# Kernel optimization log

Hardware: AMD Instinct MI355X
Metric: run time of the kernel (lower is better)

The kernel has to match this reference:

```python
import jax, jax.numpy as jnp
import numpy as np

B, T, C = 4, 2048, 1024
N_HEADS = 16
HEAD_DIM = C // N_HEADS


def setup_inputs() -> dict:
    key = jax.random.key(0)
    k1, k2, k3, k4, k5 = jax.random.split(key, 5)
    x = jax.random.normal(k1, (B, T, C), dtype=jnp.float32)
    # torch Linear: y = x @ W.T + b; store W as [out, in]
    w_qkv = jax.random.normal(k2, (3 * C, C), dtype=jnp.float32) * (1.0 / np.sqrt(C))
    b_qkv = jax.random.normal(k3, (3 * C,), dtype=jnp.float32) * 0.01
    w_proj = jax.random.normal(k4, (C, C), dtype=jnp.float32) * (1.0 / np.sqrt(C))
    b_proj = jax.random.normal(k5, (C,), dtype=jnp.float32) * 0.01
    return {"x": x, "w_qkv": w_qkv, "b_qkv": b_qkv, "w_proj": w_proj, "b_proj": b_proj}


def reference(x, w_qkv, b_qkv, w_proj, b_proj):
    Bx, Tx, Cx = x.shape
    scale = 1.0 / np.sqrt(HEAD_DIM)
    qkv = x @ w_qkv.T + b_qkv                              # [B,T,3C]
    qkv = qkv.reshape(Bx, Tx, 3, N_HEADS, HEAD_DIM)
    qkv = jnp.transpose(qkv, (2, 0, 3, 1, 4))              # [3,B,H,T,D]
    q, k, v = qkv[0], qkv[1], qkv[2]
    att = jnp.einsum('bhqd,bhkd->bhqk', q, k) * scale      # [B,H,T,T]
    causal = jnp.tril(jnp.ones((Tx, Tx), dtype=bool))
    att = jnp.where(causal[None, None, :, :], att, -jnp.inf)
    att = jax.nn.softmax(att, axis=-1)
    # dropout p=0.0 (eval) -> identity
    out = jnp.einsum('bhqk,bhkd->bhqd', att, v)            # [B,H,T,D]
    out = jnp.transpose(out, (0, 2, 1, 3)).reshape(Bx, Tx, Cx)
    return out @ w_proj.T + b_proj
```

## Files before the change

### kernel.cpp

```cpp
#include <hip/hip_runtime.h>
#include <hip/hip_bf16.h>
#include <cstdint>

typedef __attribute__((ext_vector_type(8))) short bf16x8;
typedef __attribute__((ext_vector_type(4))) float f32x4;
typedef __attribute__((ext_vector_type(16))) float f32x16;

#define MFMA16(a, b, c) __builtin_amdgcn_mfma_f32_16x16x32_bf16(a, b, c, 0, 0, 0)
#define MFMA32(a, b, c) __builtin_amdgcn_mfma_f32_32x32x16_bf16(a, b, c, 0, 0, 0)

typedef __attribute__((address_space(1))) uint32_t as1_u32;
typedef __attribute__((address_space(3))) uint32_t as3_u32;
static __device__ __forceinline__ void gload16(const void* g, void* l) {
  __builtin_amdgcn_global_load_lds((as1_u32*)g, (as3_u32*)l, 16, 0, 0);
}

static __device__ __forceinline__ ushort f2b(float f) {
  union { float f; uint32_t u; } v; v.f = f;
  uint32_t u = v.u;
  uint32_t r = (u + 0x7FFFu + ((u >> 16) & 1u)) >> 16;
  return (ushort)r;
}

static __device__ __forceinline__ uint32_t cvtpk(float a, float b) {
  uint32_t r;
  asm("v_cvt_pk_bf16_f32 %0, %1, %2" : "=v"(r) : "v"(a), "v"(b));
  return r;
}
static __device__ __forceinline__ void plswap(uint32_t& a, uint32_t& b) {
  asm volatile("v_permlane32_swap_b32 %0, %1" : "+v"(a), "+v"(b));
}

#define QSCALE 0.1803368782f

#define LOFF(r, kc4) (((r) >> 1) * 64 + ((((((r) & 1) << 2) | (kc4)) ^ (((r) >> 1) & 7)) * 8))

__global__ void cvt_f32_bf16(const float* __restrict__ in, ushort* __restrict__ out, int n4) {
  int i = blockIdx.x * blockDim.x + threadIdx.x;
  if (i >= n4) return;
  const float4 v = ((const float4*)in)[i];
  ushort4 o;
  o.x = f2b(v.x); o.y = f2b(v.y); o.z = f2b(v.z); o.w = f2b(v.w);
  ((ushort4*)out)[i] = o;
}

__global__ __launch_bounds__(512, 2) void gemm_qkv_8ph(
    const ushort* __restrict__ A,
    const ushort* __restrict__ W,
    const float* __restrict__ bias,
    int M, int N, int K,
    ushort* __restrict__ q_ws, ushort* __restrict__ k_ws, ushort* __restrict__ v_ws) {
  __shared__ ushort As[2][2][64 * 64];
  __shared__ ushort Bs[2][2][2][64 * 64];
  const int tid = threadIdx.x;
  const int cpx = gridDim.x >> 3;
  const int wg = (blockIdx.x & 7) * cpx + (blockIdx.x >> 3);
  const int m0 = (wg / 12) * 128, n0 = (wg % 12) * 256;
  const int wid = tid >> 6, lane = tid & 63;
  const int wr = wid >> 2, wc = wid & 3;
  const int lr = lane & 15, lg = lane >> 4;
  const int prow = tid >> 3, pchk = tid & 7;
  const int lchk = pchk ^ (prow & 7);
  const int srow = prow * 2 + (lchk >> 2);
  const int skc = (lchk & 3) * 8;

  f32x4 acc[4][4] = {};
  const int nt = K >> 6;

#define STA(db_, kt_)                                                         \
  { const ushort* src = A + (size_t)(m0 + srow) * K + (kt_)*64 + skc;         \
    gload16(src, &As[db_][0][tid * 8]);                                       \
    gload16(src + 32, &As[db_][1][tid * 8]); }
#define STB(db_, half_, kt_)                                                  \
  { const ushort* src = W + (size_t)(n0 + (half_)*128 + srow) * K + (kt_)*64 + skc; \
    gload16(src, &Bs[db_][half_][0][tid * 8]);                                \
    gload16(src + 32, &Bs[db_][half_][1][tid * 8]); }

  STB(0, 0, 0); STB(0, 1, 0);
  STA(0, 0);
  STB(1, 0, 1); STB(1, 1, 1);
  asm volatile("s_waitcnt vmcnt(4)" ::: "memory");
  __builtin_amdgcn_s_barrier();

  const int bhalf = wc >> 1, brow = (wc & 1) * 64;
  for (int T = 0; T < nt; ++T) {
    const int db = T & 1;
    const ushort* Asub0 = &As[db][0][0];
    const ushort* Asub1 = &As[db][1][0];
    const ushort* Bsub0 = &Bs[db][bhalf][0][0];
    const ushort* Bsub1 = &Bs[db][bhalf][1][0];
    bf16x8 b[4][2];
    {
      bf16x8 a[2][2];
#pragma unroll
      for (int mm = 0; mm < 2; ++mm) {
        const int r = wr * 64 + mm * 16 + lr;
        a[mm][0] = *(const bf16x8*)&Asub0[LOFF(r, lg)];
        a[mm][1] = *(const bf16x8*)&Asub1[LOFF(r, lg)];
      }
#pragma unroll
      for (int nf = 0; nf < 4; ++nf) {
        const int r = brow + nf * 16 + lr;
        b[nf][0] = *(const bf16x8*)&Bsub0[LOFF(r, lg)];
        b[nf][1] = *(const bf16x8*)&Bsub1[LOFF(r, lg)];
      }
      if (T + 1 < nt) STA((T + 1) & 1, T + 1);
      __builtin_amdgcn_sched_barrier(0);
      __builtin_amdgcn_s_barrier();
      asm volatile("s_waitcnt lgkmcnt(0)" ::: "memory");
      __builtin_amdgcn_sched_barrier(0);
      __builtin_amdgcn_s_setprio(1);
#pragma unroll
      for (int kk = 0; kk < 2; ++kk)
#pragma unroll
        for (int mm = 0; mm < 2; ++mm)
#pragma unroll
          for (int nf = 0; nf < 4; ++nf)
            acc[mm][nf] = MFMA16(a[mm][kk], b[nf][kk], acc[mm][nf]);
      __builtin_amdgcn_s_setprio(0);
      __builtin_amdgcn_s_barrier();
    }
    {
      bf16x8 a[2][2];
#pragma unroll
      for (int mm = 0; mm < 2; ++mm) {
        const int r = wr * 64 + (2 + mm) * 16 + lr;
        a[mm][0] = *(const bf16x8*)&Asub0[LOFF(r, lg)];
        a[mm][1] = *(const bf16x8*)&Asub1[LOFF(r, lg)];
      }
      if (T + 2 < nt) { STB(db, 0, T + 2); STB(db, 1, T + 2); }
      __builtin_amdgcn_sched_barrier(0);
      __builtin_amdgcn_s_barrier();
      asm volatile("s_waitcnt lgkmcnt(0)" ::: "memory");
      __builtin_amdgcn_sched_barrier(0);
      __builtin_amdgcn_s_setprio(1);
#pragma unroll
      for (int kk = 0; kk < 2; ++kk)
#pragma unroll
        for (int mm = 0; mm < 2; ++mm)
#pragma unroll
          for (int nf = 0; nf < 4; ++nf)
            acc[2 + mm][nf] = MFMA16(a[mm][kk], b[nf][kk], acc[2 + mm][nf]);
      __builtin_amdgcn_s_setprio(0);
      if (T + 2 < nt)
        asm volatile("s_waitcnt vmcnt(4)" ::: "memory");
      else if (T + 1 < nt)
        asm volatile("s_waitcnt vmcnt(0)" ::: "memory");
      if (T + 1 < nt) __builtin_amdgcn_s_barrier();
    }
  }
#undef STA
#undef STB

#pragma unroll
  for (int mf = 0; mf < 4; ++mf) {
#pragma unroll
    for (int nf = 0; nf < 4; ++nf) {
      const int rowb = m0 + wr * 64 + mf * 16 + lg * 4;
      const int col = n0 + wc * 64 + nf * 16 + lr;
      float v[4];
#pragma unroll
      for (int i = 0; i < 4; ++i) v[i] = acc[mf][nf][i] + bias[col];
      const int sel = col >> 10;
      const int rem = col & 1023;
      const int h = rem >> 6, d = rem & 63;
      const int bb = rowb >> 11, t0 = rowb & 2047;
      if (sel == 2) {
        ushort4 st;
        st.x = f2b(v[0]); st.y = f2b(v[1]); st.z = f2b(v[2]); st.w = f2b(v[3]);
        *(ushort4*)&v_ws[((size_t)(bb * 16 + h) * 64 + d) * 2048 + t0] = st;
      } else if (sel == 0) {
#pragma unroll
        for (int i = 0; i < 4; ++i)
          q_ws[((size_t)(bb * 16 + h) * 2048 + t0 + i) * 64 + d] = f2b(v[i] * QSCALE);
      } else {
#pragma unroll
        for (int i = 0; i < 4; ++i)
          k_ws[((size_t)(bb * 16 + h) * 2048 + t0 + i) * 64 + d] = f2b(v[i]);
      }
    }
  }
}

__global__ __launch_bounds__(256) void gemm_proj(
    const ushort* __restrict__ A,
    const ushort* __restrict__ W,
    const float* __restrict__ bias,
    int M, int N, int K,
    float* __restrict__ out) {
  __shared__ ushort As[3][64 * 64];
  __shared__ ushort Bs[3][64 * 64];
  const int tid = threadIdx.x;
  const int nbx = N >> 7;
  const int cpx = gridDim.x >> 3;
  const int wg = (blockIdx.x & 7) * cpx + (blockIdx.x >> 3);
  const int m0 = (wg / nbx) * 128, n0 = (wg % nbx) * 128;
  const int lane = tid & 63, w = tid >> 6;
  const int lr = lane & 15, lg = lane >> 4;
  const int wm = (w >> 1) * 64, wn = (w & 1) * 64;
  f32x4 acc[4][4] = {};

  const int nt = K >> 5;

#define GSTAGE(buf_, kt_)                                                   \
  do {                                                                      \
    const ushort* Asrc = A + (size_t)m0 * K + (kt_) * 32;                   \
    const ushort* Bsrc = W + (size_t)n0 * K + (kt_) * 32;                   \
    _Pragma("unroll") for (int i_ = 0; i_ < 2; ++i_) {                      \
      const int ch = i_ * 256 + tid;                                        \
      const int prow = ch >> 3, pchk = ch & 7;                              \
      const int lchk = pchk ^ (prow & 7);                                   \
      const int r = prow * 2 + (lchk >> 2), kc = (lchk & 3) * 8;            \
      gload16(&Asrc[(size_t)r * K + kc], &As[buf_][ch * 8]);                \
      gload16(&Bsrc[(size_t)r * K + kc], &Bs[buf_][ch * 8]);                \
    }                                                                       \
  } while (0)

  GSTAGE(0, 0);
  GSTAGE(1, 1);
  asm volatile("s_waitcnt vmcnt(4)" ::: "memory");
  __builtin_amdgcn_s_barrier();
  asm volatile("" ::: "memory");

  int bcur = 0, bnxt = 2;
  for (int t = 0; t < nt; ++t) {
    if (t + 2 < nt) GSTAGE(bnxt, t + 2);
    const ushort* Asc = As[bcur];
    const ushort* Bsc = Bs[bcur];
    bf16x8 a[4], b[4];
#pragma unroll
    for (int mi = 0; mi < 4; ++mi) {
      const int r = wm + mi * 16 + lr;
      a[mi] = *(const bf16x8*)&Asc[LOFF(r, lg)];
    }
#pragma unroll
    for (int ni = 0; ni < 4; ++ni) {
      const int r = wn + ni * 16 + lr;
      b[ni] = *(const bf16x8*)&Bsc[LOFF(r, lg)];
    }
    __builtin_amdgcn_s_setprio(1);
#pragma unroll
    for (int mi = 0; mi < 4; ++mi)
#pragma unroll
      for (int ni = 0; ni < 4; ++ni)
        acc[mi][ni] = MFMA16(a[mi], b[ni], acc[mi][ni]);
    __builtin_amdgcn_s_setprio(0);
    if (t + 2 < nt)
      asm volatile("s_waitcnt vmcnt(4)" ::: "memory");
    else if (t + 1 < nt)
      asm volatile("s_waitcnt vmcnt(0)" ::: "memory");
    if (t + 1 < nt) {
      __builtin_amdgcn_s_barrier();
      asm volatile("" ::: "memory");
    }
    bcur = (bcur == 2) ? 0 : bcur + 1;
    bnxt = (bnxt == 2) ? 0 : bnxt + 1;
  }
#undef GSTAGE

#pragma unroll
  for (int mi = 0; mi < 4; ++mi) {
#pragma unroll
    for (int ni = 0; ni < 4; ++ni) {
      const int rowb = m0 + wm + mi * 16 + lg * 4;
      const int col = n0 + wn + ni * 16 + lr;
#pragma unroll
      for (int i = 0; i < 4; ++i)
        out[(size_t)(rowb + i) * N + col] = acc[mi][ni][i] + bias[col];
    }
  }
}

__global__ __launch_bounds__(256) void attn_v5(
    const ushort* __restrict__ Q, const ushort* __restrict__ K,
    const ushort* __restrict__ VT, ushort* __restrict__ O ) {
  const int blk = blockIdx.x;
  const int bh = blk & 63;
  const int pr = blk >> 6;
  const int tid = threadIdx.x;
  const int w = tid >> 6, lane = tid & 63;
  const int l31 = lane & 31, l5 = lane >> 5;
  const int bb = bh >> 4, h = bh & 15;
  const size_t base = (size_t)bh * 2048 * 64;
  const ushort* Qb = Q + base;
  const ushort* Kb = K + base;
  const ushort* VTb = VT + base;

  __shared__ ushort Ks[2][64 * 64];
  __shared__ ushort Vs[2][64 * 64];
  __shared__ float l_lds[4][32];

#define STAGE(buf, kt_)                                              \
  do {                                                               \
    const ushort* Kt = Kb + (size_t)(kt_) * 64 * 64;                 \
    const ushort* Vt = VTb + (kt_) * 64;                             \
    _Pragma("unroll") for (int i_ = 0; i_ < 2; ++i_) {               \
      const int ch = i_ * 256 + tid;                                 \
      const int r = ch >> 3;                                         \
      const int csw = ((ch & 7) ^ (r & 7)) * 8;                      \
      gload16(&Kt[(size_t)r * 64 + csw], &Ks[buf][ch * 8]);          \
      gload16(&Vt[(size_t)r * 2048 + csw], &Vs[buf][ch * 8]);        \
    }                                                                \
  } while (0)

#pragma unroll 1
  for (int ph = 0; ph < 2; ++ph) {
    const int s = ph ? pr : 15 - pr;
    const int q0w = s * 128 + w * 32;
    const int nt = 2 * s + 2;
    const int qlane = q0w + l31;

    bf16x8 qf[4];
#pragma unroll
    for (int dblk = 0; dblk < 4; ++dblk)
      qf[dblk] = *(const bf16x8*)&Qb[(size_t)qlane * 64 + dblk * 16 + l5 * 8];

    f32x16 o0 = {}, o1 = {};
    float lsum = 0.f;

    STAGE(0, 0);
    __syncthreads();

    for (int kt = 0; kt < nt; ++kt) {
      const int cur = kt & 1;
      if (kt + 1 < nt) STAGE(cur ^ 1, kt + 1);
      const int k0 = kt << 6;
      const ushort* Ksc = Ks[cur];
      const ushort* Vsc = Vs[cur];
#pragma unroll
      for (int kblk = 0; kblk < 2; ++kblk) {
        const int kbase = k0 + kblk * 32;
        if (kbase <= q0w + 31) {
          f32x16 st = {};
          __builtin_amdgcn_s_setprio(1);
#pragma unroll
          for (int dblk = 0; dblk < 4; ++dblk) {
            const int row = kblk * 32 + l31;
            bf16x8 ka = *(const bf16x8*)&Ksc[row * 64 + (((dblk * 2 + l5) ^ (row & 7)) * 8)];
            st = MFMA32(ka, qf[dblk], st);
          }
          __builtin_amdgcn_s_setprio(0);
          if (kbase + 31 > q0w) {
#pragma unroll
            for (int r = 0; r < 16; ++r) {
              const int kk = kbase + (r & 3) + 8 * (r >> 2) + 4 * l5;
              st[r] = (kk <= qlane) ? st[r] : -INFINITY;
            }
          }
          float p[16];
#pragma unroll
          for (int r = 0; r < 16; ++r) {
            p[r] = __builtin_amdgcn_exp2f(st[r]);
            lsum += p[r];
          }
#pragma unroll
          for (int sbl = 0; sbl < 2; ++sbl) {
            uint32_t P0 = cvtpk(p[8 * sbl + 0], p[8 * sbl + 1]);
            uint32_t P1 = cvtpk(p[8 * sbl + 2], p[8 * sbl + 3]);
            uint32_t P2 = cvtpk(p[8 * sbl + 4], p[8 * sbl + 5]);
            uint32_t P3 = cvtpk(p[8 * sbl + 6], p[8 * sbl + 7]);
            plswap(P0, P2);
            plswap(P1, P3);
            union { uint32_t u[4]; bf16x8 v; } pk;
            pk.u[0] = P0; pk.u[1] = P1; pk.u[2] = P2; pk.u[3] = P3;
            const int kchunk = kblk * 4 + sbl * 2 + l5;
            __builtin_amdgcn_s_setprio(1);
#pragma unroll
            for (int db2 = 0; db2 < 2; ++db2) {
              const int vrow = db2 * 32 + l31;
              bf16x8 vb = *(const bf16x8*)&Vsc[vrow * 64 + ((kchunk ^ (vrow & 7)) * 8)];
              if (db2 == 0) o0 = MFMA32(pk.v, vb, o0);
              else          o1 = MFMA32(pk.v, vb, o1);
            }
            __builtin_amdgcn_s_setprio(0);
          }
        }
      }
      __syncthreads();
    }

    const float lfull = lsum + __shfl_xor(lsum, 32);
    if (lane < 32) l_lds[w][lane] = 1.f / lfull;
#pragma unroll
    for (int r = 0; r < 16; ++r) {
      const int qoff = (r & 3) + 8 * (r >> 2) + 4 * l5;
      const float inv = l_lds[w][qoff];
      const int t = q0w + qoff;
      ushort* op = &O[(size_t)(bb * 2048 + t) * 1024 + h * 64 + l31];
      op[0] = f2b(o0[r] * inv);
      op[32] = f2b(o1[r] * inv);
    }
  }
#undef STAGE
}

extern "C" void kernel_launch(void* const* d_in, const int* in_sizes, int n_in,
                              void* d_out, int out_size, void* d_ws, size_t ws_size,
                              hipStream_t stream) {
  const float* x = (const float*)d_in[0];
  const float* w_qkv = (const float*)d_in[1];
  const float* b_qkv = (const float*)d_in[2];
  const float* w_proj = (const float*)d_in[3];
  const float* b_proj = (const float*)d_in[4];
  float* out = (float*)d_out;

  char* ws = (char*)d_ws;
  const size_t SZ_X = (size_t)8192 * 1024 * 2;
  const size_t SZ_WQ = (size_t)3072 * 1024 * 2;
  const size_t SZ_WP = (size_t)1024 * 1024 * 2;
  ushort* xb = (ushort*)(ws);
  ushort* wqb = (ushort*)(ws + SZ_X);
  ushort* wpb = (ushort*)(ws + SZ_X + SZ_WQ);
  ushort* q_ws = (ushort*)(ws + SZ_X + SZ_WQ + SZ_WP);
  ushort* k_ws = q_ws + (size_t)8192 * 1024;
  ushort* v_ws = k_ws + (size_t)8192 * 1024;

  cvt_f32_bf16<<<8388608 / 4 / 256, 256, 0, stream>>>(x, xb, 8388608 / 4);
  cvt_f32_bf16<<<3145728 / 4 / 256, 256, 0, stream>>>(w_qkv, wqb, 3145728 / 4);
  cvt_f32_bf16<<<1048576 / 4 / 256, 256, 0, stream>>>(w_proj, wpb, 1048576 / 4);

  gemm_qkv_8ph<<<768, 512, 0, stream>>>(
      xb, wqb, b_qkv, 8192, 3072, 1024, q_ws, k_ws, v_ws);

  attn_v5<<<512, 256, 0, stream>>>(q_ws, k_ws, v_ws, xb);

  gemm_proj<<<512, 256, 0, stream>>>(
      xb, wpb, b_proj, 8192, 1024, 1024, out);
}
```

Baseline: 171.6 us.

## Merge conversion kernels, reuse 8-phase GEMM for projection, unpair attention blocks

The three f32-to-bf16 conversion launches become one combined kernel, which removes two launch overheads. The output projection now reuses the 512-thread, 128x256-tile templated GEMM in place of a separate 256-thread 128x128 GEMM. That gives 256 workgroups instead of 512 and drops the proj GEMM from three LDS buffers to two. The attention kernel no longer gives each block a long and a short causal query stripe. It launches 1024 blocks with one stripe each, ordered longest first, and adds a min-occupancy launch bound. This aims for better load balance and overlap, but the proj grid of 256 may leave the GPU's compute units underfilled.

```diff
diff --git a/kernel.cpp b/kernel.cpp
--- a/kernel.cpp
+++ b/kernel.cpp
@@ -35,27 +35,38 @@
 
 #define LOFF(r, kc4) (((r) >> 1) * 64 + ((((((r) & 1) << 2) | (kc4)) ^ (((r) >> 1) & 7)) * 8))
 
-__global__ void cvt_f32_bf16(const float* __restrict__ in, ushort* __restrict__ out, int n4) {
+#define N4_X  2097152
+#define N4_WQ 786432
+#define N4_WP 262144
+__global__ void cvt_all(const float* __restrict__ x, const float* __restrict__ wq,
+                        const float* __restrict__ wp, ushort* __restrict__ xb,
+                        ushort* __restrict__ wqb, ushort* __restrict__ wpb) {
   int i = blockIdx.x * blockDim.x + threadIdx.x;
-  if (i >= n4) return;
-  const float4 v = ((const float4*)in)[i];
+  const float* src; ushort* dst; int j;
+  if (i < N4_X)            { src = x;  dst = xb;  j = i; }
+  else if (i < N4_X + N4_WQ) { src = wq; dst = wqb; j = i - N4_X; }
+  else                     { src = wp; dst = wpb; j = i - (N4_X + N4_WQ); }
+  const float4 v = ((const float4*)src)[j];
   ushort4 o;
   o.x = f2b(v.x); o.y = f2b(v.y); o.z = f2b(v.z); o.w = f2b(v.w);
-  ((ushort4*)out)[i] = o;
-}
-
-__global__ __launch_bounds__(512, 2) void gemm_qkv_8ph(
+  ((ushort4*)dst)[j] = o;
+}
+
+template<int EPI>
+__global__ __launch_bounds__(512, 2) void gemm_2ph(
     const ushort* __restrict__ A,
     const ushort* __restrict__ W,
     const float* __restrict__ bias,
     int M, int N, int K,
-    ushort* __restrict__ q_ws, ushort* __restrict__ k_ws, ushort* __restrict__ v_ws) {
+    ushort* __restrict__ q_ws, ushort* __restrict__ k_ws, ushort* __restrict__ v_ws,
+    float* __restrict__ out) {
   __shared__ ushort As[2][2][64 * 64];
   __shared__ ushort Bs[2][2][2][64 * 64];
   const int tid = threadIdx.x;
+  const int nbx = N >> 8;
   const int cpx = gridDim.x >> 3;
   const int wg = (blockIdx.x & 7) * cpx + (blockIdx.x >> 3);
-  const int m0 = (wg / 12) * 128, n0 = (wg % 12) * 256;
+  const int m0 = (wg / nbx) * 128, n0 = (wg % nbx) * 256;
   const int wid = tid >> 6, lane = tid & 63;
   const int wr = wid >> 2, wc = wid & 3;
   const int lr = lane & 15, lg = lane >> 4;
@@ -161,122 +172,39 @@
       float v[4];
 #pragma unroll
       for (int i = 0; i < 4; ++i) v[i] = acc[mf][nf][i] + bias[col];
-      const int sel = col >> 10;
-      const int rem = col & 1023;
-      const int h = rem >> 6, d = rem & 63;
-      const int bb = rowb >> 11, t0 = rowb & 2047;
-      if (sel == 2) {
-        ushort4 st;
-        st.x = f2b(v[0]); st.y = f2b(v[1]); st.z = f2b(v[2]); st.w = f2b(v[3]);
-        *(ushort4*)&v_ws[((size_t)(bb * 16 + h) * 64 + d) * 2048 + t0] = st;
-      } else if (sel == 0) {
+      if (EPI == 0) {
+        const int sel = col >> 10;
+        const int rem = col & 1023;
+        const int h = rem >> 6, d = rem & 63;
+        const int bb = rowb >> 11, t0 = rowb & 2047;
+        if (sel == 2) {
+          ushort4 st;
+          st.x = f2b(v[0]); st.y = f2b(v[1]); st.z = f2b(v[2]); st.w = f2b(v[3]);
+          *(ushort4*)&v_ws[((size_t)(bb * 16 + h) * 64 + d) * 2048 + t0] = st;
+        } else if (sel == 0) {
+#pragma unroll
+          for (int i = 0; i < 4; ++i)
+            q_ws[((size_t)(bb * 16 + h) * 2048 + t0 + i) * 64 + d] = f2b(v[i] * QSCALE);
+        } else {
+#pragma unroll
+          for (int i = 0; i < 4; ++i)
+            k_ws[((size_t)(bb * 16 + h) * 2048 + t0 + i) * 64 + d] = f2b(v[i]);
+        }
+      } else {
 #pragma unroll
         for (int i = 0; i < 4; ++i)
-          q_ws[((size_t)(bb * 16 + h) * 2048 + t0 + i) * 64 + d] = f2b(v[i] * QSCALE);
-      } else {
-#pragma unroll
-        for (int i = 0; i < 4; ++i)
-          k_ws[((size_t)(bb * 16 + h) * 2048 + t0 + i) * 64 + d] = f2b(v[i]);
+          out[(size_t)(rowb + i) * N + col] = v[i];
       }
     }
   }
 }
 
-__global__ __launch_bounds__(256) void gemm_proj(
-    const ushort* __restrict__ A,
-    const ushort* __restrict__ W,
-    const float* __restrict__ bias,
-    int M, int N, int K,
-    float* __restrict__ out) {
-  __shared__ ushort As[3][64 * 64];
-  __shared__ ushort Bs[3][64 * 64];
-  const int tid = threadIdx.x;
-  const int nbx = N >> 7;
-  const int cpx = gridDim.x >> 3;
-  const int wg = (blockIdx.x & 7) * cpx + (blockIdx.x >> 3);
-  const int m0 = (wg / nbx) * 128, n0 = (wg % nbx) * 128;
-  const int lane = tid & 63, w = tid >> 6;
-  const int lr = lane & 15, lg = lane >> 4;
-  const int wm = (w >> 1) * 64, wn = (w & 1) * 64;
-  f32x4 acc[4][4] = {};
-
-  const int nt = K >> 5;
-
-#define GSTAGE(buf_, kt_)                                                   \
-  do {                                                                      \
-    const ushort* Asrc = A + (size_t)m0 * K + (kt_) * 32;                   \
-    const ushort* Bsrc = W + (size_t)n0 * K + (kt_) * 32;                   \
-    _Pragma("unroll") for (int i_ = 0; i_ < 2; ++i_) {                      \
-      const int ch = i_ * 256 + tid;                                        \
-      const int prow = ch >> 3, pchk = ch & 7;                              \
-      const int lchk = pchk ^ (prow & 7);                                   \
-      const int r = prow * 2 + (lchk >> 2), kc = (lchk & 3) * 8;            \
-      gload16(&Asrc[(size_t)r * K + kc], &As[buf_][ch * 8]);                \
-      gload16(&Bsrc[(size_t)r * K + kc], &Bs[buf_][ch * 8]);                \
-    }                                                                       \
-  } while (0)
-
-  GSTAGE(0, 0);
-  GSTAGE(1, 1);
-  asm volatile("s_waitcnt vmcnt(4)" ::: "memory");
-  __builtin_amdgcn_s_barrier();
-  asm volatile("" ::: "memory");
-
-  int bcur = 0, bnxt = 2;
-  for (int t = 0; t < nt; ++t) {
-    if (t + 2 < nt) GSTAGE(bnxt, t + 2);
-    const ushort* Asc = As[bcur];
-    const ushort* Bsc = Bs[bcur];
-    bf16x8 a[4], b[4];
-#pragma unroll
-    for (int mi = 0; mi < 4; ++mi) {
-      const int r = wm + mi * 16 + lr;
-      a[mi] = *(const bf16x8*)&Asc[LOFF(r, lg)];
-    }
-#pragma unroll
-    for (int ni = 0; ni < 4; ++ni) {
-      const int r = wn + ni * 16 + lr;
-      b[ni] = *(const bf16x8*)&Bsc[LOFF(r, lg)];
-    }
-    __builtin_amdgcn_s_setprio(1);
-#pragma unroll
-    for (int mi = 0; mi < 4; ++mi)
-#pragma unroll
-      for (int ni = 0; ni < 4; ++ni)
-        acc[mi][ni] = MFMA16(a[mi], b[ni], acc[mi][ni]);
-    __builtin_amdgcn_s_setprio(0);
-    if (t + 2 < nt)
-      asm volatile("s_waitcnt vmcnt(4)" ::: "memory");
-    else if (t + 1 < nt)
-      asm volatile("s_waitcnt vmcnt(0)" ::: "memory");
-    if (t + 1 < nt) {
-      __builtin_amdgcn_s_barrier();
-      asm volatile("" ::: "memory");
-    }
-    bcur = (bcur == 2) ? 0 : bcur + 1;
-    bnxt = (bnxt == 2) ? 0 : bnxt + 1;
-  }
-#undef GSTAGE
-
-#pragma unroll
-  for (int mi = 0; mi < 4; ++mi) {
-#pragma unroll
-    for (int ni = 0; ni < 4; ++ni) {
-      const int rowb = m0 + wm + mi * 16 + lg * 4;
-      const int col = n0 + wn + ni * 16 + lr;
-#pragma unroll
-      for (int i = 0; i < 4; ++i)
-        out[(size_t)(rowb + i) * N + col] = acc[mi][ni][i] + bias[col];
-    }
-  }
-}
-
-__global__ __launch_bounds__(256) void attn_v5(
+__global__ __launch_bounds__(256, 4) void attn_v6(
     const ushort* __restrict__ Q, const ushort* __restrict__ K,
     const ushort* __restrict__ VT, ushort* __restrict__ O ) {
   const int blk = blockIdx.x;
+  const int s = 15 - (blk >> 6);
   const int bh = blk & 63;
-  const int pr = blk >> 6;
   const int tid = threadIdx.x;
   const int w = tid >> 6, lane = tid & 63;
   const int l31 = lane & 31, l5 = lane >> 5;
@@ -303,93 +231,89 @@
     }                                                                \
   } while (0)
 
-#pragma unroll 1
-  for (int ph = 0; ph < 2; ++ph) {
-    const int s = ph ? pr : 15 - pr;
-    const int q0w = s * 128 + w * 32;
-    const int nt = 2 * s + 2;
-    const int qlane = q0w + l31;
-
-    bf16x8 qf[4];
-#pragma unroll
-    for (int dblk = 0; dblk < 4; ++dblk)
-      qf[dblk] = *(const bf16x8*)&Qb[(size_t)qlane * 64 + dblk * 16 + l5 * 8];
-
-    f32x16 o0 = {}, o1 = {};
-    float lsum = 0.f;
-
-    STAGE(0, 0);
-    __syncthreads();
-
-    for (int kt = 0; kt < nt; ++kt) {
-      const int cur = kt & 1;
-      if (kt + 1 < nt) STAGE(cur ^ 1, kt + 1);
-      const int k0 = kt << 6;
-      const ushort* Ksc = Ks[cur];
-      const ushort* Vsc = Vs[cur];
-#pragma unroll
-      for (int kblk = 0; kblk < 2; ++kblk) {
-        const int kbase = k0 + kblk * 32;
-        if (kbase <= q0w + 31) {
-          f32x16 st = {};
+  const int q0w = s * 128 + w * 32;
+  const int nt = 2 * s + 2;
+  const int qlane = q0w + l31;
+
+  bf16x8 qf[4];
+#pragma unroll
+  for (int dblk = 0; dblk < 4; ++dblk)
+    qf[dblk] = *(const bf16x8*)&Qb[(size_t)qlane * 64 + dblk * 16 + l5 * 8];
+
+  f32x16 o0 = {}, o1 = {};
+  float lsum = 0.f;
+
+  STAGE(0, 0);
+  __syncthreads();
+
+  for (int kt = 0; kt < nt; ++kt) {
+    const int cur = kt & 1;
+    if (kt + 1 < nt) STAGE(cur ^ 1, kt + 1);
+    const int k0 = kt << 6;
+    const ushort* Ksc = Ks[cur];
+    const ushort* Vsc = Vs[cur];
+#pragma unroll
+    for (int kblk = 0; kblk < 2; ++kblk) {
+      const int kbase = k0 + kblk * 32;
+      if (kbase <= q0w + 31) {
+        f32x16 st = {};
+        __builtin_amdgcn_s_setprio(1);
+#pragma unroll
+        for (int dblk = 0; dblk < 4; ++dblk) {
+          const int row = kblk * 32 + l31;
+          bf16x8 ka = *(const bf16x8*)&Ksc[row * 64 + (((dblk * 2 + l5) ^ (row & 7)) * 8)];
+          st = MFMA32(ka, qf[dblk], st);
+        }
+        __builtin_amdgcn_s_setprio(0);
+        if (kbase + 31 > q0w) {
+#pragma unroll
+          for (int r = 0; r < 16; ++r) {
+            const int kk = kbase + (r & 3) + 8 * (r >> 2) + 4 * l5;
+            st[r] = (kk <= qlane) ? st[r] : -INFINITY;
+          }
+        }
+        float p[16];
+#pragma unroll
+        for (int r = 0; r < 16; ++r) {
+          p[r] = __builtin_amdgcn_exp2f(st[r]);
+          lsum += p[r];
+        }
+#pragma unroll
+        for (int sbl = 0; sbl < 2; ++sbl) {
+          uint32_t P0 = cvtpk(p[8 * sbl + 0], p[8 * sbl + 1]);
+          uint32_t P1 = cvtpk(p[8 * sbl + 2], p[8 * sbl + 3]);
+          uint32_t P2 = cvtpk(p[8 * sbl + 4], p[8 * sbl + 5]);
+          uint32_t P3 = cvtpk(p[8 * sbl + 6], p[8 * sbl + 7]);
+          plswap(P0, P2);
+          plswap(P1, P3);
+          union { uint32_t u[4]; bf16x8 v; } pk;
+          pk.u[0] = P0; pk.u[1] = P1; pk.u[2] = P2; pk.u[3] = P3;
+          const int kchunk = kblk * 4 + sbl * 2 + l5;
           __builtin_amdgcn_s_setprio(1);
 #pragma unroll
-          for (int dblk = 0; dblk < 4; ++dblk) {
-            const int row = kblk * 32 + l31;
-            bf16x8 ka = *(const bf16x8*)&Ksc[row * 64 + (((dblk * 2 + l5) ^ (row & 7)) * 8)];
-            st = MFMA32(ka, qf[dblk], st);
+          for (int db2 = 0; db2 < 2; ++db2) {
+            const int vrow = db2 * 32 + l31;
+            bf16x8 vb = *(const bf16x8*)&Vsc[vrow * 64 + ((kchunk ^ (vrow & 7)) * 8)];
+            if (db2 == 0) o0 = MFMA32(pk.v, vb, o0);
+            else          o1 = MFMA32(pk.v, vb, o1);
           }
           __builtin_amdgcn_s_setprio(0);
-          if (kbase + 31 > q0w) {
-#pragma unroll
-            for (int r = 0; r < 16; ++r) {
-              const int kk = kbase + (r & 3) + 8 * (r >> 2) + 4 * l5;
-              st[r] = (kk <= qlane) ? st[r] : -INFINITY;
-            }
-          }
-          float p[16];
-#pragma unroll
-          for (int r = 0; r < 16; ++r) {
-            p[r] = __builtin_amdgcn_exp2f(st[r]);
-            lsum += p[r];
-          }
-#pragma unroll
-          for (int sbl = 0; sbl < 2; ++sbl) {
-            uint32_t P0 = cvtpk(p[8 * sbl + 0], p[8 * sbl + 1]);
-            uint32_t P1 = cvtpk(p[8 * sbl + 2], p[8 * sbl + 3]);
-            uint32_t P2 = cvtpk(p[8 * sbl + 4], p[8 * sbl + 5]);
-            uint32_t P3 = cvtpk(p[8 * sbl + 6], p[8 * sbl + 7]);
-            plswap(P0, P2);
-            plswap(P1, P3);
-            union { uint32_t u[4]; bf16x8 v; } pk;
-            pk.u[0] = P0; pk.u[1] = P1; pk.u[2] = P2; pk.u[3] = P3;
-            const int kchunk = kblk * 4 + sbl * 2 + l5;
-            __builtin_amdgcn_s_setprio(1);
-#pragma unroll
-            for (int db2 = 0; db2 < 2; ++db2) {
-              const int vrow = db2 * 32 + l31;
-              bf16x8 vb = *(const bf16x8*)&Vsc[vrow * 64 + ((kchunk ^ (vrow & 7)) * 8)];
-              if (db2 == 0) o0 = MFMA32(pk.v, vb, o0);
-              else          o1 = MFMA32(pk.v, vb, o1);
-            }
-            __builtin_amdgcn_s_setprio(0);
-          }
-        }
-      }
-      __syncthreads();
+        }
+      }
     }
-
-    const float lfull = lsum + __shfl_xor(lsum, 32);
-    if (lane < 32) l_lds[w][lane] = 1.f / lfull;
-#pragma unroll
-    for (int r = 0; r < 16; ++r) {
-      const int qoff = (r & 3) + 8 * (r >> 2) + 4 * l5;
-      const float inv = l_lds[w][qoff];
-      const int t = q0w + qoff;
-      ushort* op = &O[(size_t)(bb * 2048 + t) * 1024 + h * 64 + l31];
-      op[0] = f2b(o0[r] * inv);
-      op[32] = f2b(o1[r] * inv);
-    }
+    __syncthreads();
+  }
+
+  const float lfull = lsum + __shfl_xor(lsum, 32);
+  if (lane < 32) l_lds[w][lane] = 1.f / lfull;
+#pragma unroll
+  for (int r = 0; r < 16; ++r) {
+    const int qoff = (r & 3) + 8 * (r >> 2) + 4 * l5;
+    const float inv = l_lds[w][qoff];
+    const int t = q0w + qoff;
+    ushort* op = &O[(size_t)(bb * 2048 + t) * 1024 + h * 64 + l31];
+    op[0] = f2b(o0[r] * inv);
+    op[32] = f2b(o1[r] * inv);
   }
 #undef STAGE
 }
@@ -415,15 +339,14 @@
   ushort* k_ws = q_ws + (size_t)8192 * 1024;
   ushort* v_ws = k_ws + (size_t)8192 * 1024;
 
-  cvt_f32_bf16<<<8388608 / 4 / 256, 256, 0, stream>>>(x, xb, 8388608 / 4);
-  cvt_f32_bf16<<<3145728 / 4 / 256, 256, 0, stream>>>(w_qkv, wqb, 3145728 / 4);
-  cvt_f32_bf16<<<1048576 / 4 / 256, 256, 0, stream>>>(w_proj, wpb, 1048576 / 4);
-
-  gemm_qkv_8ph<<<768, 512, 0, stream>>>(
-      xb, wqb, b_qkv, 8192, 3072, 1024, q_ws, k_ws, v_ws);
-
-  attn_v5<<<512, 256, 0, stream>>>(q_ws, k_ws, v_ws, xb);
-
-  gemm_proj<<<512, 256, 0, stream>>>(
-      xb, wpb, b_proj, 8192, 1024, 1024, out);
-}
+  cvt_all<<<(N4_X + N4_WQ + N4_WP) / 256, 256, 0, stream>>>(
+      x, w_qkv, w_proj, xb, wqb, wpb);
+
+  gemm_2ph<0><<<768, 512, 0, stream>>>(
+      xb, wqb, b_qkv, 8192, 3072, 1024, q_ws, k_ws, v_ws, nullptr);
+
+  attn_v6<<<1024, 256, 0, stream>>>(q_ws, k_ws, v_ws, xb);
+
+  gemm_2ph<1><<<256, 512, 0, stream>>>(
+      xb, wpb, b_proj, 8192, 1024, 1024, nullptr, nullptr, nullptr, out);
+}
```

Measured after the change: 156.7 us. -8.7%, faster.
